# Optimization experiments

Measured on AMD Instinct MI355X. Metric: run time of the kernel, lower is better.

The kernel has to match this reference:

```python
import jax, jax.numpy as jnp
import numpy as np

CH = 128
GROUPS = 8
HEADS = 8
HEAD_DIM = CH // HEADS  # 16
EPS = 1e-5


def setup_inputs() -> dict:
    key = jax.random.key(0)
    ks = jax.random.split(key, 5)
    x = jax.random.normal(ks[0], (8, CH, 128, 128), dtype=jnp.float32)
    gn_w = jnp.ones((CH,), dtype=jnp.float32)
    gn_b = jnp.zeros((CH,), dtype=jnp.float32)
    w_in = jax.random.normal(ks[1], (CH, CH), dtype=jnp.float32) * (1.0 / np.sqrt(CH))
    b_in = jax.random.normal(ks[2], (CH,), dtype=jnp.float32) * 0.01
    w_out = jax.random.normal(ks[3], (CH, CH), dtype=jnp.float32) * (1.0 / np.sqrt(CH))
    b_out = jax.random.normal(ks[4], (CH,), dtype=jnp.float32) * 0.01
    return {"x": x, "gn_w": gn_w, "gn_b": gn_b, "w_in": w_in, "b_in": b_in,
            "w_out": w_out, "b_out": b_out}


def _group_norm(x, gamma, beta):
    b, c, H, W = x.shape
    xg = x.reshape(b, GROUPS, c // GROUPS, H, W)
    mean = xg.mean(axis=(2, 3, 4), keepdims=True)
    var = xg.var(axis=(2, 3, 4), keepdims=True)
    xg = (xg - mean) * jax.lax.rsqrt(var + EPS)
    x = xg.reshape(b, c, H, W)
    return x * gamma[None, :, None, None] + beta[None, :, None, None]


def _conv1x1(x, w, bias):
    # w: [out_c, in_c] (1x1 conv == pointwise matmul over channels)
    return jnp.einsum('oc,bchw->bohw', w, x) + bias[None, :, None, None]


def reference(x, gn_w, gn_b, w_in, b_in, w_out, b_out):
    b, c, H, W = x.shape
    h = _group_norm(x, gn_w, gn_b)
    h = _conv1x1(h, w_in, b_in)
    # reshape to [b, heads, head_dim, H*W]; attention over head_dim axis,
    # contracting the spatial axis (d = H*W) as in the original einsums
    hh = h.reshape(b, HEADS, HEAD_DIM, H * W)
    scale = HEAD_DIM ** (-0.5)
    scores = jnp.einsum('bhid,bhjd->bhij', hh, hh) * scale  # [b,heads,hd,hd]
    weights = jax.nn.softmax(scores, axis=-1)
    attn = jnp.einsum('bhij,bhjd->bhid', weights, hh)
    attn = attn.reshape(b, c, H, W)
    h = _conv1x1(attn, w_out, b_out)
    return x + h
```

## Files before the change

### kernel.cpp

```cpp
#include <hip/hip_runtime.h>


#define NPOS 16384

typedef short short8 __attribute__((ext_vector_type(8)));
typedef float f32x4 __attribute__((ext_vector_type(4)));

__device__ __forceinline__ unsigned short f2bf(float f) {
    union { float f; unsigned u; } v; v.f = f;
    unsigned r = (v.u + 0x7fffu + ((v.u >> 16) & 1u)) >> 16;
    return (unsigned short)r;
}
__device__ __forceinline__ float bf2f(unsigned short h) {
    union { unsigned u; float f; } v; v.u = ((unsigned)h) << 16;
    return v.f;
}

__global__ __launch_bounds__(256) void k_stats(const float* __restrict__ x,
                                               float* __restrict__ stats) {
    const float4* p = (const float4*)(x + (size_t)blockIdx.x * 16384);
    int t = threadIdx.x;
    float s1 = 0.f, s2 = 0.f;
#pragma unroll
    for (int j = 0; j < 16; ++j) {
        float4 v = p[t + j * 256];
        s1 += v.x + v.y + v.z + v.w;
        s2 += v.x * v.x + v.y * v.y + v.z * v.z + v.w * v.w;
    }
    for (int off = 32; off; off >>= 1) {
        s1 += __shfl_down(s1, off);
        s2 += __shfl_down(s2, off);
    }
    __shared__ float r1[4], r2[4];
    int wv = t >> 6;
    if ((t & 63) == 0) { r1[wv] = s1; r2[wv] = s2; }
    __syncthreads();
    if (t == 0) {
        s1 = r1[0] + r1[1] + r1[2] + r1[3];
        s2 = r2[0] + r2[1] + r2[2] + r2[3];
        int bg = blockIdx.x >> 4;
        atomicAdd(&stats[bg * 2 + 0], s1);
        atomicAdd(&stats[bg * 2 + 1], s2);
    }
}

__global__ __launch_bounds__(256) void k_prep(const float* __restrict__ stats,
                                              const float* __restrict__ gn_w,
                                              const float* __restrict__ gn_b,
                                              const float* __restrict__ w_in,
                                              const float* __restrict__ b_in,
                                              float* __restrict__ vA,
                                              unsigned short* __restrict__ Asb) {
    int b = blockIdx.x, t = threadIdx.x;
    __shared__ float ss[128], tl[128];
    if (t < 128) {
        int g = t >> 4;
        float s1 = stats[(b * 8 + g) * 2 + 0];
        float s2 = stats[(b * 8 + g) * 2 + 1];
        const float invN = 1.0f / 262144.0f;
        float mean = s1 * invN;
        float var = s2 * invN - mean * mean;
        float rstd = rsqrtf(var + 1e-5f);
        float s = gn_w[t] * rstd;
        ss[t] = s;
        tl[t] = gn_b[t] - mean * s;
    }
    __syncthreads();
    if (t < 128) {
        float v = b_in[t];
        const float* wr = w_in + t * 128;
#pragma unroll 8
        for (int k = 0; k < 128; ++k) v += wr[k] * tl[k];
        vA[b * 128 + t] = v;
    }
    unsigned short* ab = Asb + b * 16384;
    const float4* w4 = (const float4*)w_in;
#pragma unroll
    for (int i = 0; i < 16; ++i) {
        int idx = t + i * 256;
        int c = idx >> 5, k4 = idx & 31;
        float4 w = w4[idx];
        ushort4 o;
        o.x = f2bf(w.x * ss[k4 * 4 + 0]);
        o.y = f2bf(w.y * ss[k4 * 4 + 1]);
        o.z = f2bf(w.z * ss[k4 * 4 + 2]);
        o.w = f2bf(w.w * ss[k4 * 4 + 3]);
        *(ushort4*)&ab[c * 128 + k4 * 4] = o;
    }
}

__global__ __launch_bounds__(256, 8) void k_gemm1_scores(const float* __restrict__ x,
                                                         const unsigned short* __restrict__ Asb,
                                                         const float* __restrict__ vA,
                                                         float* __restrict__ Sg) {
    __shared__ unsigned short Xt[64 * 128];
    __shared__ float v_s[128];

    const int t = threadIdx.x;
    const int lane = t & 63, wv = t >> 6;
    const int q = lane >> 4, i16 = lane & 15;
    const int b = blockIdx.x >> 8;
    const int p0 = (blockIdx.x & 255) << 6;
    const float* xb = x + (size_t)b * (128 * NPOS) + p0;

    if (t < 128) v_s[t] = vA[b * 128 + t];

    {
        const int p = t & 63;
        const int sw = p & 15;
        const int kq0 = t >> 6;
#pragma unroll
        for (int i = 0; i < 4; ++i) {
            int kq = kq0 + i * 4;
            const float* col = xb + (size_t)(kq * 8) * NPOS + p;
            short8 o;
#pragma unroll
            for (int e = 0; e < 8; ++e)
                ((unsigned short*)&o)[e] = f2bf(col[(size_t)e * NPOS]);
            *(short8*)&Xt[p * 128 + ((kq ^ sw) << 3)] = o;
        }
    }
    __syncthreads();

    const unsigned short* ab = Asb + b * 16384;
    f32x4 acc[2][4];
#pragma unroll
    for (int a = 0; a < 2; ++a)
#pragma unroll
        for (int pt = 0; pt < 4; ++pt) acc[a][pt] = (f32x4){0.f, 0.f, 0.f, 0.f};

#pragma unroll
    for (int ks = 0; ks < 4; ++ks) {
        short8 a0 = *(const short8*)&ab[(wv * 32 + i16) * 128 + ks * 32 + q * 8];
        short8 a1 = *(const short8*)&ab[(wv * 32 + 16 + i16) * 128 + ks * 32 + q * 8];
        const int cb = ((ks * 4 + q) ^ i16) << 3;
#pragma unroll
        for (int pt = 0; pt < 4; ++pt) {
            short8 bb = *(const short8*)&Xt[(pt * 16 + i16) * 128 + cb];
            acc[0][pt] = __builtin_amdgcn_mfma_f32_16x16x32_bf16(a0, bb, acc[0][pt], 0, 0, 0);
            acc[1][pt] = __builtin_amdgcn_mfma_f32_16x16x32_bf16(a1, bb, acc[1][pt], 0, 0, 0);
        }
    }
    __syncthreads();

#pragma unroll
    for (int a = 0; a < 2; ++a) {
        int cb0 = wv * 32 + a * 16 + q * 4;
#pragma unroll
        for (int pt = 0; pt < 4; ++pt) {
            int p = pt * 16 + i16;
#pragma unroll
            for (int r = 0; r < 4; ++r) {
                int c = cb0 + r;
                Xt[c * 64 + ((((p >> 3) ^ (c & 7)) << 3)) + (p & 7)] =
                    f2bf(acc[a][pt][r] + v_s[c]);
            }
        }
    }
    __syncthreads();

#pragma unroll
    for (int hh = 0; hh < 2; ++hh) {
        int h = wv * 2 + hh;
        int row = (h * 16 + i16) * 64;
        int sw = i16 & 7;
        f32x4 sacc = (f32x4){0.f, 0.f, 0.f, 0.f};
#pragma unroll
        for (int ks = 0; ks < 2; ++ks) {
            short8 f = *(const short8*)&Xt[row + (((ks * 4 + q) ^ sw) << 3)];
            sacc = __builtin_amdgcn_mfma_f32_16x16x32_bf16(f, f, sacc, 0, 0, 0);
        }
        float* sg = Sg + (b * 8 + h) * 256;
#pragma unroll
        for (int r = 0; r < 4; ++r)
            atomicAdd(&sg[(q * 4 + r) * 16 + i16], sacc[r]);
    }
}

__global__ __launch_bounds__(256) void k_softmax_weff(const float* __restrict__ Sg,
                                                      const float* __restrict__ w_out,
                                                      unsigned short* __restrict__ weffb) {
    int b = blockIdx.x, t = threadIdx.x;
    __shared__ float W[2048];
    if (t < 128) {
        const float* row = Sg + b * 2048 + t * 16;
        float v[16];
        float m = -1e30f;
#pragma unroll
        for (int j = 0; j < 16; ++j) { v[j] = row[j] * 0.25f; m = fmaxf(m, v[j]); }
        float sum = 0.f;
#pragma unroll
        for (int j = 0; j < 16; ++j) { v[j] = __expf(v[j] - m); sum += v[j]; }
        float inv = 1.0f / sum;
#pragma unroll
        for (int j = 0; j < 16; ++j) W[t * 16 + j] = v[j] * inv;
    }
    __syncthreads();
    unsigned short* wo = weffb + b * 16384;
#pragma unroll 2
    for (int n = 0; n < 64; ++n) {
        int idx = t + n * 256;
        int c = idx >> 7, k = idx & 127;
        int h = k >> 4, j = k & 15;
        const float* wr = w_out + c * 128 + h * 16;
        const float* Wr = W + h * 256 + j;
        float a = 0.f;
#pragma unroll
        for (int i = 0; i < 16; ++i) a += wr[i] * Wr[i * 16];
        wo[idx] = f2bf(a);
    }
}

__global__ __launch_bounds__(256, 6) void k_attn_out(const float* __restrict__ x,
                                                     const unsigned short* __restrict__ Asb,
                                                     const float* __restrict__ vA,
                                                     const unsigned short* __restrict__ weffb,
                                                     const float* __restrict__ b_out,
                                                     float* __restrict__ out) {
    __shared__ unsigned short Xt[64 * 128];
    __shared__ float v_s[128];
    __shared__ float bo_s[128];

    const int t = threadIdx.x;
    const int lane = t & 63, wv = t >> 6;
    const int q = lane >> 4, i16 = lane & 15;
    const int b = blockIdx.x >> 8;
    const int p0 = (blockIdx.x & 255) << 6;
    const float* xb = x + (size_t)b * (128 * NPOS) + p0;

    if (t < 128) { v_s[t] = vA[b * 128 + t]; bo_s[t] = b_out[t]; }

    {
        const int p = t & 63;
        const int sw = p & 15;
        const int kq0 = t >> 6;
#pragma unroll
        for (int i = 0; i < 4; ++i) {
            int kq = kq0 + i * 4;
            const float* col = xb + (size_t)(kq * 8) * NPOS + p;
            short8 o;
#pragma unroll
            for (int e = 0; e < 8; ++e)
                ((unsigned short*)&o)[e] = f2bf(col[(size_t)e * NPOS]);
            *(short8*)&Xt[p * 128 + ((kq ^ sw) << 3)] = o;
        }
    }
    __syncthreads();

    const unsigned short* ab = Asb + b * 16384;
    f32x4 acc1[2][4];
#pragma unroll
    for (int a = 0; a < 2; ++a)
#pragma unroll
        for (int pt = 0; pt < 4; ++pt) acc1[a][pt] = (f32x4){0.f, 0.f, 0.f, 0.f};

#pragma unroll
    for (int ks = 0; ks < 4; ++ks) {
        short8 a0 = *(const short8*)&ab[(wv * 32 + i16) * 128 + ks * 32 + q * 8];
        short8 a1 = *(const short8*)&ab[(wv * 32 + 16 + i16) * 128 + ks * 32 + q * 8];
        const int cb = ((ks * 4 + q) ^ i16) << 3;
#pragma unroll
        for (int pt = 0; pt < 4; ++pt) {
            short8 bb = *(const short8*)&Xt[(pt * 16 + i16) * 128 + cb];
            acc1[0][pt] = __builtin_amdgcn_mfma_f32_16x16x32_bf16(a0, bb, acc1[0][pt], 0, 0, 0);
            acc1[1][pt] = __builtin_amdgcn_mfma_f32_16x16x32_bf16(a1, bb, acc1[1][pt], 0, 0, 0);
        }
    }
    __syncthreads();

#pragma unroll
    for (int a = 0; a < 2; ++a) {
        int cb0 = wv * 32 + a * 16 + q * 4;
#pragma unroll
        for (int pt = 0; pt < 4; ++pt) {
            int p = pt * 16 + i16;
#pragma unroll
            for (int r = 0; r < 4; ++r) {
                int c = cb0 + r;
                Xt[p * 128 + ((((c >> 3) ^ i16) << 3)) + (c & 7)] =
                    f2bf(acc1[a][pt][r] + v_s[c]);
            }
        }
    }
    __syncthreads();

    const unsigned short* ab2 = weffb + b * 16384;
    f32x4 acc2[2][4];
#pragma unroll
    for (int a = 0; a < 2; ++a)
#pragma unroll
        for (int pt = 0; pt < 4; ++pt) acc2[a][pt] = (f32x4){0.f, 0.f, 0.f, 0.f};

#pragma unroll
    for (int ks = 0; ks < 4; ++ks) {
        short8 a0 = *(const short8*)&ab2[(wv * 32 + i16) * 128 + ks * 32 + q * 8];
        short8 a1 = *(const short8*)&ab2[(wv * 32 + 16 + i16) * 128 + ks * 32 + q * 8];
        const int cb = ((ks * 4 + q) ^ i16) << 3;
#pragma unroll
        for (int pt = 0; pt < 4; ++pt) {
            short8 bb = *(const short8*)&Xt[(pt * 16 + i16) * 128 + cb];
            acc2[0][pt] = __builtin_amdgcn_mfma_f32_16x16x32_bf16(a0, bb, acc2[0][pt], 0, 0, 0);
            acc2[1][pt] = __builtin_amdgcn_mfma_f32_16x16x32_bf16(a1, bb, acc2[1][pt], 0, 0, 0);
        }
    }
    __syncthreads();

#pragma unroll
    for (int a = 0; a < 2; ++a) {
        int cb0 = wv * 32 + a * 16 + q * 4;
#pragma unroll
        for (int pt = 0; pt < 4; ++pt) {
            int p = pt * 16 + i16;
#pragma unroll
            for (int r = 0; r < 4; ++r) {
                int c = cb0 + r;
                Xt[c * 64 + ((((p >> 3) ^ (c & 7)) << 3)) + (p & 7)] =
                    f2bf(acc2[a][pt][r] + bo_s[c]);
            }
        }
    }
    __syncthreads();

    float* ob = out + (size_t)b * (128 * NPOS) + p0;
#pragma unroll
    for (int i = 0; i < 8; ++i) {
        int idx = t + i * 256;
        int c = idx >> 4, pc4 = idx & 15;
        int p = pc4 * 4;
        ushort4 hv = *(const ushort4*)&Xt[c * 64 + ((((p >> 3) ^ (c & 7)) << 3)) + (p & 7)];
        const float4 xv = *(const float4*)&xb[(size_t)c * NPOS + p];
        float4 o;
        o.x = xv.x + bf2f(hv.x);
        o.y = xv.y + bf2f(hv.y);
        o.z = xv.z + bf2f(hv.z);
        o.w = xv.w + bf2f(hv.w);
        *(float4*)&ob[(size_t)c * NPOS + p] = o;
    }
}

extern "C" void kernel_launch(void* const* d_in, const int* in_sizes, int n_in,
                              void* d_out, int out_size, void* d_ws, size_t ws_size,
                              hipStream_t stream) {
    const float* x    = (const float*)d_in[0];
    const float* gn_w = (const float*)d_in[1];
    const float* gn_b = (const float*)d_in[2];
    const float* w_in = (const float*)d_in[3];
    const float* b_in = (const float*)d_in[4];
    const float* w_out= (const float*)d_in[5];
    const float* b_out= (const float*)d_in[6];
    float* out = (float*)d_out;

    float* ws    = (float*)d_ws;
    float* stats = ws;
    float* Sg    = ws + 128;
    float* vA    = ws + 16512;
    unsigned short* Asb   = (unsigned short*)(ws + 17536);
    unsigned short* weffb = (unsigned short*)(ws + 83072);

    hipMemsetAsync(d_ws, 0, (128 + 16384) * sizeof(float), stream);
    k_stats<<<dim3(1024), dim3(256), 0, stream>>>(x, stats);
    k_prep<<<dim3(8), dim3(256), 0, stream>>>(stats, gn_w, gn_b, w_in, b_in, vA, Asb);
    k_gemm1_scores<<<dim3(2048), dim3(256), 0, stream>>>(x, Asb, vA, Sg);
    k_softmax_weff<<<dim3(8), dim3(256), 0, stream>>>(Sg, w_out, weffb);
    k_attn_out<<<dim3(2048), dim3(256), 0, stream>>>(x, Asb, vA, weffb, b_out, out);
}
```

Before: 210.0 us.

## Compute scores from input Gram matrix, dropping the separate GEMM1 pass

New measurement: 373.6 us. 77.9% more time.

```diff
diff --git a/kernel.cpp b/kernel.cpp
--- a/kernel.cpp
+++ b/kernel.cpp
@@ -16,85 +16,274 @@
     return v.f;
 }
 
-__global__ __launch_bounds__(256) void k_stats(const float* __restrict__ x,
-                                               float* __restrict__ stats) {
-    const float4* p = (const float4*)(x + (size_t)blockIdx.x * 16384);
-    int t = threadIdx.x;
-    float s1 = 0.f, s2 = 0.f;
-#pragma unroll
-    for (int j = 0; j < 16; ++j) {
-        float4 v = p[t + j * 256];
-        s1 += v.x + v.y + v.z + v.w;
-        s2 += v.x * v.x + v.y * v.y + v.z * v.z + v.w * v.w;
-    }
-    for (int off = 32; off; off >>= 1) {
-        s1 += __shfl_down(s1, off);
-        s2 += __shfl_down(s2, off);
-    }
-    __shared__ float r1[4], r2[4];
-    int wv = t >> 6;
-    if ((t & 63) == 0) { r1[wv] = s1; r2[wv] = s2; }
-    __syncthreads();
-    if (t == 0) {
-        s1 = r1[0] + r1[1] + r1[2] + r1[3];
-        s2 = r2[0] + r2[1] + r2[2] + r2[3];
-        int bg = blockIdx.x >> 4;
-        atomicAdd(&stats[bg * 2 + 0], s1);
-        atomicAdd(&stats[bg * 2 + 1], s2);
-    }
-}
-
-__global__ __launch_bounds__(256) void k_prep(const float* __restrict__ stats,
-                                              const float* __restrict__ gn_w,
-                                              const float* __restrict__ gn_b,
-                                              const float* __restrict__ w_in,
-                                              const float* __restrict__ b_in,
-                                              float* __restrict__ vA,
-                                              unsigned short* __restrict__ Asb) {
-    int b = blockIdx.x, t = threadIdx.x;
-    __shared__ float ss[128], tl[128];
-    if (t < 128) {
-        int g = t >> 4;
-        float s1 = stats[(b * 8 + g) * 2 + 0];
-        float s2 = stats[(b * 8 + g) * 2 + 1];
+__global__ __launch_bounds__(256) void k_gram(const float* __restrict__ x,
+                                              float* __restrict__ Gws) {
+    __shared__ unsigned short Xs[2][8192];
+
+    const int t = threadIdx.x;
+    const int lane = t & 63, wv = t >> 6;
+    const int q = lane >> 4, i16 = lane & 15;
+    const int b = blockIdx.x >> 5;
+    const int slab0 = (blockIdx.x & 31) << 9;
+    const float* xb = x + (size_t)b * (128 * NPOS) + slab0;
+
+    const int pc = t & 7;
+    const int kr0 = t >> 3;
+
+    short8 ones;
+#pragma unroll
+    for (int e = 0; e < 8; ++e) ((unsigned short*)&ones)[e] = 0x3F80;
+
+    f32x4 acc[2][8];
+    f32x4 ao[2];
+#pragma unroll
+    for (int i2 = 0; i2 < 2; ++i2) {
+        ao[i2] = (f32x4){0.f, 0.f, 0.f, 0.f};
+#pragma unroll
+        for (int j = 0; j < 8; ++j) acc[i2][j] = (f32x4){0.f, 0.f, 0.f, 0.f};
+    }
+
+#pragma unroll
+    for (int i = 0; i < 4; ++i) {
+        int k = kr0 + i * 32;
+        const float4* src = (const float4*)(xb + (size_t)k * NPOS + pc * 8);
+        float4 v0 = src[0], v1 = src[1];
+        short8 o;
+        ((unsigned short*)&o)[0] = f2bf(v0.x); ((unsigned short*)&o)[1] = f2bf(v0.y);
+        ((unsigned short*)&o)[2] = f2bf(v0.z); ((unsigned short*)&o)[3] = f2bf(v0.w);
+        ((unsigned short*)&o)[4] = f2bf(v1.x); ((unsigned short*)&o)[5] = f2bf(v1.y);
+        ((unsigned short*)&o)[6] = f2bf(v1.z); ((unsigned short*)&o)[7] = f2bf(v1.w);
+        *(short8*)&Xs[0][k * 64 + ((pc ^ (k & 7)) << 3)] = o;
+    }
+    __syncthreads();
+
+    for (int cc = 0; cc < 8; ++cc) {
+        if (cc < 7) {
+            int bf = (cc + 1) & 1;
+            int pbase = (cc + 1) * 64 + pc * 8;
+#pragma unroll
+            for (int i = 0; i < 4; ++i) {
+                int k = kr0 + i * 32;
+                const float4* src = (const float4*)(xb + (size_t)k * NPOS + pbase);
+                float4 v0 = src[0], v1 = src[1];
+                short8 o;
+                ((unsigned short*)&o)[0] = f2bf(v0.x); ((unsigned short*)&o)[1] = f2bf(v0.y);
+                ((unsigned short*)&o)[2] = f2bf(v0.z); ((unsigned short*)&o)[3] = f2bf(v0.w);
+                ((unsigned short*)&o)[4] = f2bf(v1.x); ((unsigned short*)&o)[5] = f2bf(v1.y);
+                ((unsigned short*)&o)[6] = f2bf(v1.z); ((unsigned short*)&o)[7] = f2bf(v1.w);
+                *(short8*)&Xs[bf][k * 64 + ((pc ^ (k & 7)) << 3)] = o;
+            }
+        }
+        const unsigned short* Xb = Xs[cc & 1];
+#pragma unroll
+        for (int kk = 0; kk < 2; ++kk) {
+            short8 f[8];
+#pragma unroll
+            for (int r = 0; r < 8; ++r) {
+                int row = r * 16 + i16;
+                f[r] = *(const short8*)&Xb[row * 64 + (((kk * 4 + q) ^ (row & 7)) << 3)];
+            }
+#pragma unroll
+            for (int i2 = 0; i2 < 2; ++i2) {
+                short8 fa = f[wv * 2 + i2];
+                ao[i2] = __builtin_amdgcn_mfma_f32_16x16x32_bf16(fa, ones, ao[i2], 0, 0, 0);
+#pragma unroll
+                for (int j = 0; j < 8; ++j)
+                    acc[i2][j] = __builtin_amdgcn_mfma_f32_16x16x32_bf16(fa, f[j], acc[i2][j], 0, 0, 0);
+            }
+        }
+        __syncthreads();
+    }
+
+    float* Gb = Gws + b * 16512;
+#pragma unroll
+    for (int i2 = 0; i2 < 2; ++i2) {
+        int rbase = (wv * 2 + i2) * 16 + q * 4;
+#pragma unroll
+        for (int j = 0; j < 8; ++j)
+#pragma unroll
+            for (int r = 0; r < 4; ++r)
+                atomicAdd(&Gb[(rbase + r) * 128 + j * 16 + i16], acc[i2][j][r]);
+        if (i16 == 0)
+#pragma unroll
+            for (int r = 0; r < 4; ++r)
+                atomicAdd(&Gb[16384 + rbase + r], ao[i2][r]);
+    }
+}
+
+__global__ __launch_bounds__(256) void k_prep2(const float* __restrict__ Gws,
+                                               const float* __restrict__ gn_w,
+                                               const float* __restrict__ gn_b,
+                                               const float* __restrict__ w_in,
+                                               const float* __restrict__ b_in,
+                                               const float* __restrict__ w_out,
+                                               float* __restrict__ vA,
+                                               unsigned short* __restrict__ Asb,
+                                               unsigned short* __restrict__ weffb) {
+    __shared__ float s_l[128], t_l[128], v_l[128], u_l[128];
+    __shared__ float tmpA[128], tmpB[128], red[16];
+    __shared__ unsigned short As_l[16384];
+    __shared__ unsigned short Gb_l[16384];
+    __shared__ unsigned short Pb_l[16384];
+    __shared__ float Wl[2048];
+
+    const int t = threadIdx.x;
+    const int lane = t & 63, wv = t >> 6;
+    const int q = lane >> 4, i16 = lane & 15;
+    const int b = blockIdx.x;
+    const float* Gb = Gws + b * 16512;
+    const float* Rb = Gb + 16384;
+
+    if (t < 128) { tmpA[t] = Gb[t * 128 + t]; tmpB[t] = Rb[t]; }
+    __syncthreads();
+    if (t < 8) {
+        float s2 = 0.f, s1 = 0.f;
+#pragma unroll
+        for (int k = 0; k < 16; ++k) { s2 += tmpA[t * 16 + k]; s1 += tmpB[t * 16 + k]; }
         const float invN = 1.0f / 262144.0f;
         float mean = s1 * invN;
         float var = s2 * invN - mean * mean;
-        float rstd = rsqrtf(var + 1e-5f);
-        float s = gn_w[t] * rstd;
-        ss[t] = s;
-        tl[t] = gn_b[t] - mean * s;
+        red[t] = mean;
+        red[8 + t] = rsqrtf(var + 1e-5f);
     }
     __syncthreads();
     if (t < 128) {
-        float v = b_in[t];
+        int g = t >> 4;
+        float s = gn_w[t] * red[8 + g];
+        s_l[t] = s;
+        t_l[t] = gn_b[t] - red[g] * s;
+    }
+    __syncthreads();
+    if (t < 128) {
+        float v = b_in[t], u = 0.f;
         const float* wr = w_in + t * 128;
 #pragma unroll 8
-        for (int k = 0; k < 128; ++k) v += wr[k] * tl[k];
+        for (int k = 0; k < 128; ++k) {
+            float w = wr[k];
+            v += w * t_l[k];
+            u += w * s_l[k] * tmpB[k];
+        }
+        v_l[t] = v; u_l[t] = u;
         vA[b * 128 + t] = v;
     }
-    unsigned short* ab = Asb + b * 16384;
-    const float4* w4 = (const float4*)w_in;
-#pragma unroll
-    for (int i = 0; i < 16; ++i) {
-        int idx = t + i * 256;
-        int c = idx >> 5, k4 = idx & 31;
-        float4 w = w4[idx];
-        ushort4 o;
-        o.x = f2bf(w.x * ss[k4 * 4 + 0]);
-        o.y = f2bf(w.y * ss[k4 * 4 + 1]);
-        o.z = f2bf(w.z * ss[k4 * 4 + 2]);
-        o.w = f2bf(w.w * ss[k4 * 4 + 3]);
-        *(ushort4*)&ab[c * 128 + k4 * 4] = o;
-    }
-}
-
-__global__ __launch_bounds__(256, 8) void k_gemm1_scores(const float* __restrict__ x,
-                                                         const unsigned short* __restrict__ Asb,
-                                                         const float* __restrict__ vA,
-                                                         float* __restrict__ Sg) {
-    __shared__ unsigned short Xt[64 * 128];
+    __syncthreads();
+
+    {
+        const float4* w4 = (const float4*)w_in;
+        const float4* g4 = (const float4*)Gb;
+        unsigned short* abg = Asb + b * 16384;
+#pragma unroll
+        for (int rep = 0; rep < 16; ++rep) {
+            int idx4 = t + rep * 256;
+            int c = idx4 >> 5, k0 = (idx4 & 31) * 4;
+            int addr = c * 128 + ((((k0 >> 3) ^ (c & 7)) << 3)) + (k0 & 7);
+            float4 w = w4[idx4];
+            ushort4 o;
+            o.x = f2bf(w.x * s_l[k0 + 0]); o.y = f2bf(w.y * s_l[k0 + 1]);
+            o.z = f2bf(w.z * s_l[k0 + 2]); o.w = f2bf(w.w * s_l[k0 + 3]);
+            *(ushort4*)&As_l[addr] = o;
+            *(ushort4*)&abg[c * 128 + k0] = o;
+            float4 g = g4[idx4];
+            ushort4 og;
+            og.x = f2bf(g.x); og.y = f2bf(g.y); og.z = f2bf(g.z); og.w = f2bf(g.w);
+            *(ushort4*)&Gb_l[addr] = og;
+        }
+    }
+    __syncthreads();
+
+    {
+        f32x4 pacc[2][8];
+#pragma unroll
+        for (int i2 = 0; i2 < 2; ++i2)
+#pragma unroll
+            for (int j = 0; j < 8; ++j) pacc[i2][j] = (f32x4){0.f, 0.f, 0.f, 0.f};
+#pragma unroll
+        for (int kk = 0; kk < 4; ++kk) {
+            int ch = ((kk * 4 + q) ^ (i16 & 7)) << 3;
+            short8 fa[2], fb[8];
+#pragma unroll
+            for (int i2 = 0; i2 < 2; ++i2)
+                fa[i2] = *(const short8*)&As_l[((wv * 2 + i2) * 16 + i16) * 128 + ch];
+#pragma unroll
+            for (int j = 0; j < 8; ++j)
+                fb[j] = *(const short8*)&Gb_l[(j * 16 + i16) * 128 + ch];
+#pragma unroll
+            for (int i2 = 0; i2 < 2; ++i2)
+#pragma unroll
+                for (int j = 0; j < 8; ++j)
+                    pacc[i2][j] = __builtin_amdgcn_mfma_f32_16x16x32_bf16(fa[i2], fb[j], pacc[i2][j], 0, 0, 0);
+        }
+#pragma unroll
+        for (int i2 = 0; i2 < 2; ++i2) {
+#pragma unroll
+            for (int j = 0; j < 8; ++j) {
+#pragma unroll
+                for (int r = 0; r < 4; ++r) {
+                    int c = (wv * 2 + i2) * 16 + q * 4 + r;
+                    int l = j * 16 + i16;
+                    Pb_l[c * 128 + ((((l >> 3) ^ (c & 7)) << 3)) + (l & 7)] = f2bf(pacc[i2][j][r]);
+                }
+            }
+        }
+    }
+    __syncthreads();
+
+#pragma unroll
+    for (int hh = 0; hh < 2; ++hh) {
+        int h = wv * 2 + hh;
+        f32x4 sacc = (f32x4){0.f, 0.f, 0.f, 0.f};
+#pragma unroll
+        for (int kk = 0; kk < 4; ++kk) {
+            int ch = ((kk * 4 + q) ^ (i16 & 7)) << 3;
+            short8 fa = *(const short8*)&Pb_l[(h * 16 + i16) * 128 + ch];
+            short8 fb = *(const short8*)&As_l[(h * 16 + i16) * 128 + ch];
+            sacc = __builtin_amdgcn_mfma_f32_16x16x32_bf16(fa, fb, sacc, 0, 0, 0);
+        }
+        int cn = h * 16 + i16;
+#pragma unroll
+        for (int r = 0; r < 4; ++r) {
+            int cm = h * 16 + q * 4 + r;
+            float L = 0.25f * (sacc[r] + v_l[cm] * u_l[cn] + u_l[cm] * v_l[cn]
+                               + 16384.f * v_l[cm] * v_l[cn]);
+            float m = L;
+#pragma unroll
+            for (int d = 1; d < 16; d <<= 1) m = fmaxf(m, __shfl_xor(m, d, 16));
+            float e = __expf(L - m);
+            float sum = e;
+#pragma unroll
+            for (int d = 1; d < 16; d <<= 1) sum += __shfl_xor(sum, d, 16);
+            Wl[(h * 16 + q * 4 + r) * 16 + i16] = e / sum;
+        }
+    }
+    __syncthreads();
+
+    {
+        unsigned short* wo = weffb + b * 16384;
+#pragma unroll 2
+        for (int rep = 0; rep < 64; ++rep) {
+            int idx = t + rep * 256;
+            int c = idx >> 7, col = idx & 127;
+            int h = col >> 4, n = col & 15;
+            const float* wr = w_out + c * 128 + h * 16;
+            const float* Wr = Wl + h * 256 + n;
+            float a = 0.f;
+#pragma unroll
+            for (int m = 0; m < 16; ++m) a += wr[m] * Wr[m * 16];
+            wo[idx] = f2bf(a);
+        }
+    }
+}
+
+__global__ __launch_bounds__(256, 4) void k_out(const float* __restrict__ x,
+                                                const unsigned short* __restrict__ Asb,
+                                                const float* __restrict__ vA,
+                                                const unsigned short* __restrict__ weffb,
+                                                const float* __restrict__ b_out,
+                                                float* __restrict__ out) {
+    __shared__ unsigned short Xs[8192];
+    __shared__ unsigned short Ht[8192];
     __shared__ float v_s[128];
+    __shared__ float bo_s[128];
 
     const int t = threadIdx.x;
     const int lane = t & 63, wv = t >> 6;
@@ -103,7 +292,7 @@
     const int p0 = (blockIdx.x & 255) << 6;
     const float* xb = x + (size_t)b * (128 * NPOS) + p0;
 
-    if (t < 128) v_s[t] = vA[b * 128 + t];
+    if (t < 128) { v_s[t] = vA[b * 128 + t]; bo_s[t] = b_out[t]; }
 
     {
         const int p = t & 63;
@@ -117,17 +306,17 @@
 #pragma unroll
             for (int e = 0; e < 8; ++e)
                 ((unsigned short*)&o)[e] = f2bf(col[(size_t)e * NPOS]);
-            *(short8*)&Xt[p * 128 + ((kq ^ sw) << 3)] = o;
+            *(short8*)&Xs[p * 128 + ((kq ^ sw) << 3)] = o;
         }
     }
     __syncthreads();
 
     const unsigned short* ab = Asb + b * 16384;
-    f32x4 acc[2][4];
+    f32x4 acc1[2][4];
 #pragma unroll
     for (int a = 0; a < 2; ++a)
 #pragma unroll
-        for (int pt = 0; pt < 4; ++pt) acc[a][pt] = (f32x4){0.f, 0.f, 0.f, 0.f};
+        for (int pt = 0; pt < 4; ++pt) acc1[a][pt] = (f32x4){0.f, 0.f, 0.f, 0.f};
 
 #pragma unroll
     for (int ks = 0; ks < 4; ++ks) {
@@ -136,12 +325,11 @@
         const int cb = ((ks * 4 + q) ^ i16) << 3;
 #pragma unroll
         for (int pt = 0; pt < 4; ++pt) {
-            short8 bb = *(const short8*)&Xt[(pt * 16 + i16) * 128 + cb];
-            acc[0][pt] = __builtin_amdgcn_mfma_f32_16x16x32_bf16(a0, bb, acc[0][pt], 0, 0, 0);
-            acc[1][pt] = __builtin_amdgcn_mfma_f32_16x16x32_bf16(a1, bb, acc[1][pt], 0, 0, 0);
-        }
-    }
-    __syncthreads();
+            short8 bb = *(const short8*)&Xs[(pt * 16 + i16) * 128 + cb];
+            acc1[0][pt] = __builtin_amdgcn_mfma_f32_16x16x32_bf16(a0, bb, acc1[0][pt], 0, 0, 0);
+            acc1[1][pt] = __builtin_amdgcn_mfma_f32_16x16x32_bf16(a1, bb, acc1[1][pt], 0, 0, 0);
+        }
+    }
 
 #pragma unroll
     for (int a = 0; a < 2; ++a) {
@@ -152,132 +340,7 @@
 #pragma unroll
             for (int r = 0; r < 4; ++r) {
                 int c = cb0 + r;
-                Xt[c * 64 + ((((p >> 3) ^ (c & 7)) << 3)) + (p & 7)] =
-                    f2bf(acc[a][pt][r] + v_s[c]);
-            }
-        }
-    }
-    __syncthreads();
-
-#pragma unroll
-    for (int hh = 0; hh < 2; ++hh) {
-        int h = wv * 2 + hh;
-        int row = (h * 16 + i16) * 64;
-        int sw = i16 & 7;
-        f32x4 sacc = (f32x4){0.f, 0.f, 0.f, 0.f};
-#pragma unroll
-        for (int ks = 0; ks < 2; ++ks) {
-            short8 f = *(const short8*)&Xt[row + (((ks * 4 + q) ^ sw) << 3)];
-            sacc = __builtin_amdgcn_mfma_f32_16x16x32_bf16(f, f, sacc, 0, 0, 0);
-        }
-        float* sg = Sg + (b * 8 + h) * 256;
-#pragma unroll
-        for (int r = 0; r < 4; ++r)
-            atomicAdd(&sg[(q * 4 + r) * 16 + i16], sacc[r]);
-    }
-}
-
-__global__ __launch_bounds__(256) void k_softmax_weff(const float* __restrict__ Sg,
-                                                      const float* __restrict__ w_out,
-                                                      unsigned short* __restrict__ weffb) {
-    int b = blockIdx.x, t = threadIdx.x;
-    __shared__ float W[2048];
-    if (t < 128) {
-        const float* row = Sg + b * 2048 + t * 16;
-        float v[16];
-        float m = -1e30f;
-#pragma unroll
-        for (int j = 0; j < 16; ++j) { v[j] = row[j] * 0.25f; m = fmaxf(m, v[j]); }
-        float sum = 0.f;
-#pragma unroll
-        for (int j = 0; j < 16; ++j) { v[j] = __expf(v[j] - m); sum += v[j]; }
-        float inv = 1.0f / sum;
-#pragma unroll
-        for (int j = 0; j < 16; ++j) W[t * 16 + j] = v[j] * inv;
-    }
-    __syncthreads();
-    unsigned short* wo = weffb + b * 16384;
-#pragma unroll 2
-    for (int n = 0; n < 64; ++n) {
-        int idx = t + n * 256;
-        int c = idx >> 7, k = idx & 127;
-        int h = k >> 4, j = k & 15;
-        const float* wr = w_out + c * 128 + h * 16;
-        const float* Wr = W + h * 256 + j;
-        float a = 0.f;
-#pragma unroll
-        for (int i = 0; i < 16; ++i) a += wr[i] * Wr[i * 16];
-        wo[idx] = f2bf(a);
-    }
-}
-
-__global__ __launch_bounds__(256, 6) void k_attn_out(const float* __restrict__ x,
-                                                     const unsigned short* __restrict__ Asb,
-                                                     const float* __restrict__ vA,
-                                                     const unsigned short* __restrict__ weffb,
-                                                     const float* __restrict__ b_out,
-                                                     float* __restrict__ out) {
-    __shared__ unsigned short Xt[64 * 128];
-    __shared__ float v_s[128];
-    __shared__ float bo_s[128];
-
-    const int t = threadIdx.x;
-    const int lane = t & 63, wv = t >> 6;
-    const int q = lane >> 4, i16 = lane & 15;
-    const int b = blockIdx.x >> 8;
-    const int p0 = (blockIdx.x & 255) << 6;
-    const float* xb = x + (size_t)b * (128 * NPOS) + p0;
-
-    if (t < 128) { v_s[t] = vA[b * 128 + t]; bo_s[t] = b_out[t]; }
-
-    {
-        const int p = t & 63;
-        const int sw = p & 15;
-        const int kq0 = t >> 6;
-#pragma unroll
-        for (int i = 0; i < 4; ++i) {
-            int kq = kq0 + i * 4;
-            const float* col = xb + (size_t)(kq * 8) * NPOS + p;
-            short8 o;
-#pragma unroll
-            for (int e = 0; e < 8; ++e)
-                ((unsigned short*)&o)[e] = f2bf(col[(size_t)e * NPOS]);
-            *(short8*)&Xt[p * 128 + ((kq ^ sw) << 3)] = o;
-        }
-    }
-    __syncthreads();
-
-    const unsigned short* ab = Asb + b * 16384;
-    f32x4 acc1[2][4];
-#pragma unroll
-    for (int a = 0; a < 2; ++a)
-#pragma unroll
-        for (int pt = 0; pt < 4; ++pt) acc1[a][pt] = (f32x4){0.f, 0.f, 0.f, 0.f};
-
-#pragma unroll
-    for (int ks = 0; ks < 4; ++ks) {
-        short8 a0 = *(const short8*)&ab[(wv * 32 + i16) * 128 + ks * 32 + q * 8];
-        short8 a1 = *(const short8*)&ab[(wv * 32 + 16 + i16) * 128 + ks * 32 + q * 8];
-        const int cb = ((ks * 4 + q) ^ i16) << 3;
-#pragma unroll
-        for (int pt = 0; pt < 4; ++pt) {
-            short8 bb = *(const short8*)&Xt[(pt * 16 + i16) * 128 + cb];
-            acc1[0][pt] = __builtin_amdgcn_mfma_f32_16x16x32_bf16(a0, bb, acc1[0][pt], 0, 0, 0);
-            acc1[1][pt] = __builtin_amdgcn_mfma_f32_16x16x32_bf16(a1, bb, acc1[1][pt], 0, 0, 0);
-        }
-    }
-    __syncthreads();
-
-#pragma unroll
-    for (int a = 0; a < 2; ++a) {
-        int cb0 = wv * 32 + a * 16 + q * 4;
-#pragma unroll
-        for (int pt = 0; pt < 4; ++pt) {
-            int p = pt * 16 + i16;
-#pragma unroll
-            for (int r = 0; r < 4; ++r) {
-                int c = cb0 + r;
-                Xt[p * 128 + ((((c >> 3) ^ i16) << 3)) + (c & 7)] =
+                Ht[p * 128 + ((((c >> 3) ^ i16) << 3)) + (c & 7)] =
                     f2bf(acc1[a][pt][r] + v_s[c]);
             }
         }
@@ -298,7 +361,7 @@
         const int cb = ((ks * 4 + q) ^ i16) << 3;
 #pragma unroll
         for (int pt = 0; pt < 4; ++pt) {
-            short8 bb = *(const short8*)&Xt[(pt * 16 + i16) * 128 + cb];
+            short8 bb = *(const short8*)&Ht[(pt * 16 + i16) * 128 + cb];
             acc2[0][pt] = __builtin_amdgcn_mfma_f32_16x16x32_bf16(a0, bb, acc2[0][pt], 0, 0, 0);
             acc2[1][pt] = __builtin_amdgcn_mfma_f32_16x16x32_bf16(a1, bb, acc2[1][pt], 0, 0, 0);
         }
@@ -314,7 +377,7 @@
 #pragma unroll
             for (int r = 0; r < 4; ++r) {
                 int c = cb0 + r;
-                Xt[c * 64 + ((((p >> 3) ^ (c & 7)) << 3)) + (p & 7)] =
+                Ht[c * 64 + ((((p >> 3) ^ (c & 7)) << 3)) + (p & 7)] =
                     f2bf(acc2[a][pt][r] + bo_s[c]);
             }
         }
@@ -325,15 +388,14 @@
 #pragma unroll
     for (int i = 0; i < 8; ++i) {
         int idx = t + i * 256;
-        int c = idx >> 4, pc4 = idx & 15;
-        int p = pc4 * 4;
-        ushort4 hv = *(const ushort4*)&Xt[c * 64 + ((((p >> 3) ^ (c & 7)) << 3)) + (p & 7)];
-        const float4 xv = *(const float4*)&xb[(size_t)c * NPOS + p];
+        int c = idx >> 4, p4 = idx & 15;
+        int p = p4 * 4;
+        ushort4 hv = *(const ushort4*)&Ht[c * 64 + ((((p >> 3) ^ (c & 7)) << 3)) + (p & 7)];
         float4 o;
-        o.x = xv.x + bf2f(hv.x);
-        o.y = xv.y + bf2f(hv.y);
-        o.z = xv.z + bf2f(hv.z);
-        o.w = xv.w + bf2f(hv.w);
+        o.x = bf2f(Xs[(p + 0) * 128 + ((((c >> 3) ^ ((p + 0) & 15)) << 3)) + (c & 7)]) + bf2f(hv.x);
+        o.y = bf2f(Xs[(p + 1) * 128 + ((((c >> 3) ^ ((p + 1) & 15)) << 3)) + (c & 7)]) + bf2f(hv.y);
+        o.z = bf2f(Xs[(p + 2) * 128 + ((((c >> 3) ^ ((p + 2) & 15)) << 3)) + (c & 7)]) + bf2f(hv.z);
+        o.w = bf2f(Xs[(p + 3) * 128 + ((((c >> 3) ^ ((p + 3) & 15)) << 3)) + (c & 7)]) + bf2f(hv.w);
         *(float4*)&ob[(size_t)c * NPOS + p] = o;
     }
 }
@@ -350,17 +412,15 @@
     const float* b_out= (const float*)d_in[6];
     float* out = (float*)d_out;
 
-    float* ws    = (float*)d_ws;
-    float* stats = ws;
-    float* Sg    = ws + 128;
-    float* vA    = ws + 16512;
-    unsigned short* Asb   = (unsigned short*)(ws + 17536);
-    unsigned short* weffb = (unsigned short*)(ws + 83072);
-
-    hipMemsetAsync(d_ws, 0, (128 + 16384) * sizeof(float), stream);
-    k_stats<<<dim3(1024), dim3(256), 0, stream>>>(x, stats);
-    k_prep<<<dim3(8), dim3(256), 0, stream>>>(stats, gn_w, gn_b, w_in, b_in, vA, Asb);
-    k_gemm1_scores<<<dim3(2048), dim3(256), 0, stream>>>(x, Asb, vA, Sg);
-    k_softmax_weff<<<dim3(8), dim3(256), 0, stream>>>(Sg, w_out, weffb);
-    k_attn_out<<<dim3(2048), dim3(256), 0, stream>>>(x, Asb, vA, weffb, b_out, out);
-}
+    float* ws = (float*)d_ws;
+    float* Gws = ws;
+    float* vA  = ws + 132096;
+    unsigned short* Asb   = (unsigned short*)(ws + 133120);
+    unsigned short* weffb = (unsigned short*)(ws + 198656);
+
+    hipMemsetAsync(d_ws, 0, 132096 * sizeof(float), stream);
+    k_gram<<<dim3(256), dim3(256), 0, stream>>>(x, Gws);
+    k_prep2<<<dim3(8), dim3(256), 0, stream>>>(Gws, gn_w, gn_b, w_in, b_in, w_out,
+                                               vA, Asb, weffb);
+    k_out<<<dim3(2048), dim3(256), 0, stream>>>(x, Asb, vA, weffb, b_out, out);
+}
```
